# Optimization experiments

Measured on AMD Instinct MI355X. Metric: run time of the kernel, lower is better.

The kernel has to match this reference:

```python
import jax, jax.numpy as jnp
import numpy as np

N_NODES = 100000
N_EDGES = 1600000
NFEAT = 256
NHID = 128


def setup_inputs() -> dict:
    key = jax.random.key(0)
    ks = jax.random.split(key, 8)
    x = jax.random.normal(ks[0], (N_NODES, NFEAT), dtype=jnp.float32)
    edge_row = jax.random.randint(ks[1], (N_EDGES,), 0, N_NODES, dtype=jnp.int32)
    edge_col = jax.random.randint(ks[2], (N_EDGES,), 0, N_NODES, dtype=jnp.int32)
    edge_val = jax.random.uniform(ks[3], (N_EDGES,), dtype=jnp.float32)
    # Glorot-ish init for the two GraphConvolution weights
    W1 = jax.random.normal(ks[4], (NFEAT, NHID), dtype=jnp.float32) * (1.0 / np.sqrt(NFEAT))
    b1 = jnp.zeros((NHID,), dtype=jnp.float32)
    W2 = jax.random.normal(ks[5], (NHID, NHID), dtype=jnp.float32) * (1.0 / np.sqrt(NHID))
    b2 = jnp.zeros((NHID,), dtype=jnp.float32)
    return {"x": x, "edge_row": edge_row, "edge_col": edge_col,
            "edge_val": edge_val, "W1": W1, "b1": b1, "W2": W2, "b2": b2}


def _gcn_layer(h, W, b, edge_row, edge_col, edge_val, n_nodes):
    # support = h @ W  (dense transform), then spmm(adj, support) + b
    support = h @ W                              # [N, d_out]
    msgs = edge_val[:, None] * support[edge_col]  # [E, d_out] gather
    agg = jax.ops.segment_sum(msgs, edge_row, num_segments=n_nodes)  # scatter-add
    return agg + b


def reference(x, edge_row, edge_col, edge_val, W1, b1, W2, b2):
    n = x.shape[0]
    # eval mode: dropout is identity
    h = jax.nn.relu(_gcn_layer(x, W1, b1, edge_row, edge_col, edge_val, n))
    for _ in range(4):  # gc2 applied 4 times with shared weights
        h = jax.nn.relu(_gcn_layer(h, W2, b2, edge_row, edge_col, edge_val, n))
    return h
```

## Files before the change

kernel.cpp:

```cpp
#include <hip/hip_runtime.h>

constexpr int NFEAT = 256;
constexpr int NHID  = 128;
constexpr int SCAN_B = 4096;


__global__ void hist_kernel(const int* __restrict__ rows, int* __restrict__ cnt,
                            int* __restrict__ rank, int n) {
  int i = blockIdx.x * blockDim.x + threadIdx.x;
  if (i < n) rank[i] = atomicAdd(&cnt[rows[i]], 1);
}

__global__ void scan1_kernel(const int* __restrict__ cnt, int* __restrict__ part,
                             int* __restrict__ bsum, int n) {
  __shared__ int tmp[1024];
  int tid = threadIdx.x;
  int base = blockIdx.x * SCAN_B + tid * 4;
  int4 v = make_int4(0, 0, 0, 0);
  if (base + 4 <= n) {
    v = *(const int4*)&cnt[base];
  } else {
    if (base + 0 < n) v.x = cnt[base + 0];
    if (base + 1 < n) v.y = cnt[base + 1];
    if (base + 2 < n) v.z = cnt[base + 2];
    if (base + 3 < n) v.w = cnt[base + 3];
  }
  int s = v.x + v.y + v.z + v.w;
  tmp[tid] = s;
  __syncthreads();
  for (int off = 1; off < 1024; off <<= 1) {
    int t = (tid >= off) ? tmp[tid - off] : 0;
    __syncthreads();
    tmp[tid] += t;
    __syncthreads();
  }
  int excl = tmp[tid] - s;
  if (base + 0 < n) part[base + 0] = excl;
  if (base + 1 < n) part[base + 1] = excl + v.x;
  if (base + 2 < n) part[base + 2] = excl + v.x + v.y;
  if (base + 3 < n) part[base + 3] = excl + v.x + v.y + v.z;
  if (tid == 1023) bsum[blockIdx.x] = tmp[1023];
}

__global__ void scan2_kernel(int* __restrict__ bsum, int nb) {
  if (threadIdx.x == 0 && blockIdx.x == 0) {
    int run = 0;
    for (int i = 0; i < nb; ++i) { int t = bsum[i]; bsum[i] = run; run += t; }
    bsum[nb] = run;
  }
}

__global__ void scan3_kernel(int* __restrict__ row_ptr, const int* __restrict__ bsum,
                             int n, int nb) {
  int i = blockIdx.x * blockDim.x + threadIdx.x;
  if (i < n) row_ptr[i] += bsum[i / SCAN_B];
  if (i == 0) row_ptr[n] = bsum[nb];
}

__global__ void scatter_kernel(const int* __restrict__ rows, const int* __restrict__ cols,
                               const float* __restrict__ vals, const int* __restrict__ rank,
                               const int* __restrict__ row_ptr, int2* __restrict__ ev_s, int n) {
  int i = blockIdx.x * blockDim.x + threadIdx.x;
  if (i < n) {
    int p = row_ptr[rows[i]] + rank[i];
    ev_s[p] = make_int2(cols[i], __float_as_int(vals[i]));
  }
}


__device__ __forceinline__ void gload16(const float* src, float* dst_lds) {
  __builtin_amdgcn_global_load_lds(
      (const __attribute__((address_space(1))) void*)src,
      (__attribute__((address_space(3))) void*)dst_lds,
      16, 0, 0);
}

template<int K>
__global__ __launch_bounds__(256) void gemm_kernel(const float* __restrict__ A,
                                                   const float* __restrict__ W,
                                                   float* __restrict__ C, int M) {
  __shared__ __align__(16) float As[2][2048];
  __shared__ __align__(16) float Bs[2][2048];
  const int tid  = threadIdx.x;
  const int w    = tid >> 6;
  const int lane = tid & 63;
  const int r8   = tid >> 4;
  const int c8   = tid & 15;
  const int block_row = blockIdx.x * 128;

  float acc[2][2][4][4] = {};

  auto prefetch = [&](int t) {
    const int buf = t & 1;
    const int k0  = t * 16;
    #pragma unroll
    for (int j = 0; j < 2; ++j) {
      int s   = j * 256 + w * 64 + lane;
      int row = s >> 2;
      int q   = (s & 3) ^ ((row >> 2) & 3);
      int grow = block_row + row;
      if (grow >= M) grow = M - 1;
      gload16(A + (size_t)grow * K + k0 + q * 4,
              &As[buf][(j * 256 + w * 64) * 4]);
    }
    #pragma unroll
    for (int j = 0; j < 2; ++j) {
      int s = j * 256 + w * 64 + lane;
      int r = s >> 5, cq = s & 31;
      gload16(W + (size_t)(k0 + r) * 128 + cq * 4,
              &Bs[buf][(j * 256 + w * 64) * 4]);
    }
  };

  constexpr int NT = K / 16;
  prefetch(0);
  for (int t = 0; t < NT; ++t) {
    __syncthreads();
    if (t + 1 < NT) prefetch(t + 1);
    const float* as = As[t & 1];
    const float* bs = Bs[t & 1];
    #pragma unroll
    for (int q = 0; q < 4; ++q) {
      float av[2][4][4];
      #pragma unroll
      for (int rh = 0; rh < 2; ++rh)
        #pragma unroll
        for (int i = 0; i < 4; ++i) {
          int row = rh * 64 + r8 * 4 + i;
          float4 a = *(const float4*)&as[(row * 4 + (q ^ ((row >> 2) & 3))) * 4];
          av[rh][i][0] = a.x; av[rh][i][1] = a.y;
          av[rh][i][2] = a.z; av[rh][i][3] = a.w;
        }
      #pragma unroll
      for (int j = 0; j < 4; ++j) {
        int kk = q * 4 + j;
        float4 b0 = *(const float4*)&bs[(kk * 32 + c8) * 4];
        float4 b1 = *(const float4*)&bs[(kk * 32 + 16 + c8) * 4];
        #pragma unroll
        for (int rh = 0; rh < 2; ++rh)
          #pragma unroll
          for (int i = 0; i < 4; ++i) {
            float a = av[rh][i][j];
            acc[rh][0][i][0] += a * b0.x; acc[rh][0][i][1] += a * b0.y;
            acc[rh][0][i][2] += a * b0.z; acc[rh][0][i][3] += a * b0.w;
            acc[rh][1][i][0] += a * b1.x; acc[rh][1][i][1] += a * b1.y;
            acc[rh][1][i][2] += a * b1.z; acc[rh][1][i][3] += a * b1.w;
          }
      }
    }
  }

  #pragma unroll
  for (int rh = 0; rh < 2; ++rh)
    #pragma unroll
    for (int i = 0; i < 4; ++i) {
      int grow = block_row + rh * 64 + r8 * 4 + i;
      if (grow < M) {
        #pragma unroll
        for (int ch = 0; ch < 2; ++ch) {
          float4 v = make_float4(acc[rh][ch][i][0], acc[rh][ch][i][1],
                                 acc[rh][ch][i][2], acc[rh][ch][i][3]);
          *(float4*)&C[(size_t)grow * 128 + ch * 64 + c8 * 4] = v;
        }
      }
    }
}


__global__ void spmm_kernel(const float* __restrict__ support, const int* __restrict__ row_ptr,
                            const int2* __restrict__ ev, const float* __restrict__ bias,
                            float* __restrict__ out, int n_nodes) {
  int wid   = blockIdx.x * (blockDim.x >> 6) + (threadIdx.x >> 6);
  int lane  = threadIdx.x & 63;
  int half  = lane >> 5;
  int flane = lane & 31;
  int row   = wid * 2 + half;
  bool rv   = row < n_nodes;
  int beg = rv ? row_ptr[row]     : 0;
  int end = rv ? row_ptr[row + 1] : 0;
  int deg = end - beg;
  int mdeg = max(__shfl(deg, 0), __shfl(deg, 32));

  float4 acc = make_float4(0.f, 0.f, 0.f, 0.f);
  const int sb = half * 32;

  for (int chunk = 0; chunk < mdeg; chunk += 32) {
    int idx = beg + chunk + flane;
    int2 ee = (idx < end) ? ev[idx] : make_int2(0, 0);
    int   cl = ee.x;
    float vl = __int_as_float(ee.y);
    int m = min(32, mdeg - chunk);
    int e = 0;
    for (; e + 8 <= m; e += 8) {
      int   c0 = __shfl(cl, sb + e + 0), c1 = __shfl(cl, sb + e + 1);
      int   c2 = __shfl(cl, sb + e + 2), c3 = __shfl(cl, sb + e + 3);
      int   c4 = __shfl(cl, sb + e + 4), c5 = __shfl(cl, sb + e + 5);
      int   c6 = __shfl(cl, sb + e + 6), c7 = __shfl(cl, sb + e + 7);
      float v0 = __shfl(vl, sb + e + 0), v1 = __shfl(vl, sb + e + 1);
      float v2 = __shfl(vl, sb + e + 2), v3 = __shfl(vl, sb + e + 3);
      float v4 = __shfl(vl, sb + e + 4), v5 = __shfl(vl, sb + e + 5);
      float v6 = __shfl(vl, sb + e + 6), v7 = __shfl(vl, sb + e + 7);
      float4 s0 = *(const float4*)&support[(size_t)c0 * 128 + flane * 4];
      float4 s1 = *(const float4*)&support[(size_t)c1 * 128 + flane * 4];
      float4 s2 = *(const float4*)&support[(size_t)c2 * 128 + flane * 4];
      float4 s3 = *(const float4*)&support[(size_t)c3 * 128 + flane * 4];
      float4 s4 = *(const float4*)&support[(size_t)c4 * 128 + flane * 4];
      float4 s5 = *(const float4*)&support[(size_t)c5 * 128 + flane * 4];
      float4 s6 = *(const float4*)&support[(size_t)c6 * 128 + flane * 4];
      float4 s7 = *(const float4*)&support[(size_t)c7 * 128 + flane * 4];
      acc.x += v0 * s0.x; acc.y += v0 * s0.y; acc.z += v0 * s0.z; acc.w += v0 * s0.w;
      acc.x += v1 * s1.x; acc.y += v1 * s1.y; acc.z += v1 * s1.z; acc.w += v1 * s1.w;
      acc.x += v2 * s2.x; acc.y += v2 * s2.y; acc.z += v2 * s2.z; acc.w += v2 * s2.w;
      acc.x += v3 * s3.x; acc.y += v3 * s3.y; acc.z += v3 * s3.z; acc.w += v3 * s3.w;
      acc.x += v4 * s4.x; acc.y += v4 * s4.y; acc.z += v4 * s4.z; acc.w += v4 * s4.w;
      acc.x += v5 * s5.x; acc.y += v5 * s5.y; acc.z += v5 * s5.z; acc.w += v5 * s5.w;
      acc.x += v6 * s6.x; acc.y += v6 * s6.y; acc.z += v6 * s6.z; acc.w += v6 * s6.w;
      acc.x += v7 * s7.x; acc.y += v7 * s7.y; acc.z += v7 * s7.z; acc.w += v7 * s7.w;
    }
    for (; e < m; ++e) {
      int   ce = __shfl(cl, sb + e);
      float ve = __shfl(vl, sb + e);
      float4 s = *(const float4*)&support[(size_t)ce * 128 + flane * 4];
      acc.x += ve * s.x; acc.y += ve * s.y; acc.z += ve * s.z; acc.w += ve * s.w;
    }
  }
  if (rv) {
    float4 b = *(const float4*)&bias[flane * 4];
    float4 o = make_float4(fmaxf(acc.x + b.x, 0.f), fmaxf(acc.y + b.y, 0.f),
                           fmaxf(acc.z + b.z, 0.f), fmaxf(acc.w + b.w, 0.f));
    *(float4*)&out[(size_t)row * 128 + flane * 4] = o;
  }
}


extern "C" void kernel_launch(void* const* d_in, const int* in_sizes, int n_in,
                              void* d_out, int out_size, void* d_ws, size_t ws_size,
                              hipStream_t stream) {
  const float* x    = (const float*)d_in[0];
  const int*   erow = (const int*)d_in[1];
  const int*   ecol = (const int*)d_in[2];
  const float* evl  = (const float*)d_in[3];
  const float* W1   = (const float*)d_in[4];
  const float* b1   = (const float*)d_in[5];
  const float* W2   = (const float*)d_in[6];
  const float* b2   = (const float*)d_in[7];
  int n_nodes = in_sizes[0] / NFEAT;
  int n_edges = in_sizes[1];
  float* out = (float*)d_out;

  char* ws = (char*)d_ws;
  size_t off = 0;
  auto alloc = [&](size_t bytes) -> void* {
    void* p = ws + off;
    off += bytes;
    off = (off + 255) & ~(size_t)255;
    return p;
  };
  float* support = (float*)alloc((size_t)n_nodes * NHID * sizeof(float));
  int*   cnt     = (int*)alloc((size_t)n_nodes * sizeof(int));
  int*   row_ptr = (int*)alloc(((size_t)n_nodes + 1) * sizeof(int));
  int*   rank    = (int*)alloc((size_t)n_edges * sizeof(int));
  int2*  ev_s    = (int2*)alloc((size_t)n_edges * sizeof(int2));
  int nb = (n_nodes + SCAN_B - 1) / SCAN_B;
  int*   bsum    = (int*)alloc((size_t)(nb + 1) * sizeof(int));

  hipMemsetAsync(cnt, 0, (size_t)n_nodes * sizeof(int), stream);
  hist_kernel<<<(n_edges + 255) / 256, 256, 0, stream>>>(erow, cnt, rank, n_edges);
  scan1_kernel<<<nb, 1024, 0, stream>>>(cnt, row_ptr, bsum, n_nodes);
  scan2_kernel<<<1, 64, 0, stream>>>(bsum, nb);
  scan3_kernel<<<(n_nodes + 255) / 256, 256, 0, stream>>>(row_ptr, bsum, n_nodes, nb);
  scatter_kernel<<<(n_edges + 255) / 256, 256, 0, stream>>>(erow, ecol, evl, rank,
                                                            row_ptr, ev_s, n_edges);

  int gblocks = (n_nodes + 127) / 128;
  int sblocks = (n_nodes + 7) / 8;

  gemm_kernel<NFEAT><<<gblocks, 256, 0, stream>>>(x, W1, support, n_nodes);
  spmm_kernel<<<sblocks, 256, 0, stream>>>(support, row_ptr, ev_s, b1, out, n_nodes);

  for (int l = 0; l < 4; ++l) {
    gemm_kernel<NHID><<<gblocks, 256, 0, stream>>>(out, W2, support, n_nodes);
    spmm_kernel<<<sblocks, 256, 0, stream>>>(support, row_ptr, ev_s, b2, out, n_nodes);
  }
}
```

Baseline: 980.0 us.

## Sort rows by degree for balanced SpMM and unroll gather loop by 16

Adds a counting sort of rows by in-degree (histogram, reverse scan, scatter into a row permutation) so each wavefront's two half-wave rows have similar degree, which reduces divergence caused by padding to the larger degree. The SpMM kernel now reads its row through the permutation and gains a 16-wide unrolled gather loop to keep more loads in flight. The cost is three extra setup kernels, an extra indirection per row, and output writes and row_ptr reads that are no longer in row order. The wider unroll also raises register pressure.

```diff
diff --git a/kernel.cpp b/kernel.cpp
--- a/kernel.cpp
+++ b/kernel.cpp
@@ -3,6 +3,7 @@
 constexpr int NFEAT = 256;
 constexpr int NHID  = 128;
 constexpr int SCAN_B = 4096;
+constexpr int DBINS  = 256;
 
 
 __global__ void hist_kernel(const int* __restrict__ rows, int* __restrict__ cnt,
@@ -64,6 +65,43 @@
   if (i < n) {
     int p = row_ptr[rows[i]] + rank[i];
     ev_s[p] = make_int2(cols[i], __float_as_int(vals[i]));
+  }
+}
+
+
+__global__ void deg_hist_kernel(const int* __restrict__ deg, int* __restrict__ dbins, int n) {
+  __shared__ int h[DBINS];
+  int tid = threadIdx.x;
+  if (tid < DBINS) h[tid] = 0;
+  __syncthreads();
+  for (int i = blockIdx.x * blockDim.x + tid; i < n; i += gridDim.x * blockDim.x)
+    atomicAdd(&h[min(deg[i], DBINS - 1)], 1);
+  __syncthreads();
+  if (tid < DBINS) atomicAdd(&dbins[tid], h[tid]);
+}
+
+__global__ void deg_scan_kernel(const int* __restrict__ dbins, int* __restrict__ dcur) {
+  __shared__ int tmp[DBINS];
+  int tid = threadIdx.x;
+  int rb  = DBINS - 1 - tid;
+  int v = dbins[rb];
+  tmp[tid] = v;
+  __syncthreads();
+  for (int off = 1; off < DBINS; off <<= 1) {
+    int t = (tid >= off) ? tmp[tid - off] : 0;
+    __syncthreads();
+    tmp[tid] += t;
+    __syncthreads();
+  }
+  dcur[rb] = tmp[tid] - v;
+}
+
+__global__ void deg_scatter_kernel(const int* __restrict__ deg, int* __restrict__ dcur,
+                                   int* __restrict__ rowperm, int n) {
+  int i = blockIdx.x * blockDim.x + threadIdx.x;
+  if (i < n) {
+    int pos = atomicAdd(&dcur[min(deg[i], DBINS - 1)], 1);
+    rowperm[pos] = i;
   }
 }
 
@@ -168,17 +206,19 @@
 
 
 __global__ void spmm_kernel(const float* __restrict__ support, const int* __restrict__ row_ptr,
-                            const int2* __restrict__ ev, const float* __restrict__ bias,
-                            float* __restrict__ out, int n_nodes) {
+                            const int2* __restrict__ ev, const int* __restrict__ rowperm,
+                            const float* __restrict__ bias, float* __restrict__ out,
+                            int n_nodes) {
   int wid   = blockIdx.x * (blockDim.x >> 6) + (threadIdx.x >> 6);
   int lane  = threadIdx.x & 63;
   int half  = lane >> 5;
   int flane = lane & 31;
-  int row   = wid * 2 + half;
-  bool rv   = row < n_nodes;
+  int pidx  = wid * 2 + half;
+  bool rv   = pidx < n_nodes;
+  int row   = rv ? rowperm[pidx] : 0;
   int beg = rv ? row_ptr[row]     : 0;
   int end = rv ? row_ptr[row + 1] : 0;
-  int deg = end - beg;
+  int deg = rv ? (end - beg) : 0;
   int mdeg = max(__shfl(deg, 0), __shfl(deg, 32));
 
   float4 acc = make_float4(0.f, 0.f, 0.f, 0.f);
@@ -191,6 +231,56 @@
     float vl = __int_as_float(ee.y);
     int m = min(32, mdeg - chunk);
     int e = 0;
+    for (; e + 16 <= m; e += 16) {
+      int   c0 = __shfl(cl, sb + e + 0),  c1 = __shfl(cl, sb + e + 1);
+      int   c2 = __shfl(cl, sb + e + 2),  c3 = __shfl(cl, sb + e + 3);
+      int   c4 = __shfl(cl, sb + e + 4),  c5 = __shfl(cl, sb + e + 5);
+      int   c6 = __shfl(cl, sb + e + 6),  c7 = __shfl(cl, sb + e + 7);
+      int   c8 = __shfl(cl, sb + e + 8),  c9 = __shfl(cl, sb + e + 9);
+      int   cA = __shfl(cl, sb + e + 10), cB = __shfl(cl, sb + e + 11);
+      int   cC = __shfl(cl, sb + e + 12), cD = __shfl(cl, sb + e + 13);
+      int   cE = __shfl(cl, sb + e + 14), cF = __shfl(cl, sb + e + 15);
+      float v0 = __shfl(vl, sb + e + 0),  v1 = __shfl(vl, sb + e + 1);
+      float v2 = __shfl(vl, sb + e + 2),  v3 = __shfl(vl, sb + e + 3);
+      float v4 = __shfl(vl, sb + e + 4),  v5 = __shfl(vl, sb + e + 5);
+      float v6 = __shfl(vl, sb + e + 6),  v7 = __shfl(vl, sb + e + 7);
+      float v8 = __shfl(vl, sb + e + 8),  v9 = __shfl(vl, sb + e + 9);
+      float vA = __shfl(vl, sb + e + 10), vB = __shfl(vl, sb + e + 11);
+      float vC = __shfl(vl, sb + e + 12), vD = __shfl(vl, sb + e + 13);
+      float vE = __shfl(vl, sb + e + 14), vF = __shfl(vl, sb + e + 15);
+      float4 s0 = *(const float4*)&support[(size_t)c0 * 128 + flane * 4];
+      float4 s1 = *(const float4*)&support[(size_t)c1 * 128 + flane * 4];
+      float4 s2 = *(const float4*)&support[(size_t)c2 * 128 + flane * 4];
+      float4 s3 = *(const float4*)&support[(size_t)c3 * 128 + flane * 4];
+      float4 s4 = *(const float4*)&support[(size_t)c4 * 128 + flane * 4];
+      float4 s5 = *(const float4*)&support[(size_t)c5 * 128 + flane * 4];
+      float4 s6 = *(const float4*)&support[(size_t)c6 * 128 + flane * 4];
+      float4 s7 = *(const float4*)&support[(size_t)c7 * 128 + flane * 4];
+      float4 s8 = *(const float4*)&support[(size_t)c8 * 128 + flane * 4];
+      float4 s9 = *(const float4*)&support[(size_t)c9 * 128 + flane * 4];
+      float4 sA = *(const float4*)&support[(size_t)cA * 128 + flane * 4];
+      float4 sB = *(const float4*)&support[(size_t)cB * 128 + flane * 4];
+      float4 sC = *(const float4*)&support[(size_t)cC * 128 + flane * 4];
+      float4 sD = *(const float4*)&support[(size_t)cD * 128 + flane * 4];
+      float4 sE = *(const float4*)&support[(size_t)cE * 128 + flane * 4];
+      float4 sF = *(const float4*)&support[(size_t)cF * 128 + flane * 4];
+      acc.x += v0 * s0.x; acc.y += v0 * s0.y; acc.z += v0 * s0.z; acc.w += v0 * s0.w;
+      acc.x += v1 * s1.x; acc.y += v1 * s1.y; acc.z += v1 * s1.z; acc.w += v1 * s1.w;
+      acc.x += v2 * s2.x; acc.y += v2 * s2.y; acc.z += v2 * s2.z; acc.w += v2 * s2.w;
+      acc.x += v3 * s3.x; acc.y += v3 * s3.y; acc.z += v3 * s3.z; acc.w += v3 * s3.w;
+      acc.x += v4 * s4.x; acc.y += v4 * s4.y; acc.z += v4 * s4.z; acc.w += v4 * s4.w;
+      acc.x += v5 * s5.x; acc.y += v5 * s5.y; acc.z += v5 * s5.z; acc.w += v5 * s5.w;
+      acc.x += v6 * s6.x; acc.y += v6 * s6.y; acc.z += v6 * s6.z; acc.w += v6 * s6.w;
+      acc.x += v7 * s7.x; acc.y += v7 * s7.y; acc.z += v7 * s7.z; acc.w += v7 * s7.w;
+      acc.x += v8 * s8.x; acc.y += v8 * s8.y; acc.z += v8 * s8.z; acc.w += v8 * s8.w;
+      acc.x += v9 * s9.x; acc.y += v9 * s9.y; acc.z += v9 * s9.z; acc.w += v9 * s9.w;
+      acc.x += vA * sA.x; acc.y += vA * sA.y; acc.z += vA * sA.z; acc.w += vA * sA.w;
+      acc.x += vB * sB.x; acc.y += vB * sB.y; acc.z += vB * sB.z; acc.w += vB * sB.w;
+      acc.x += vC * sC.x; acc.y += vC * sC.y; acc.z += vC * sC.z; acc.w += vC * sC.w;
+      acc.x += vD * sD.x; acc.y += vD * sD.y; acc.z += vD * sD.z; acc.w += vD * sD.w;
+      acc.x += vE * sE.x; acc.y += vE * sE.y; acc.z += vE * sE.z; acc.w += vE * sE.w;
+      acc.x += vF * sF.x; acc.y += vF * sF.y; acc.z += vF * sF.z; acc.w += vF * sF.w;
+    }
     for (; e + 8 <= m; e += 8) {
       int   c0 = __shfl(cl, sb + e + 0), c1 = __shfl(cl, sb + e + 1);
       int   c2 = __shfl(cl, sb + e + 2), c3 = __shfl(cl, sb + e + 3);
@@ -261,25 +351,32 @@
   int*   row_ptr = (int*)alloc(((size_t)n_nodes + 1) * sizeof(int));
   int*   rank    = (int*)alloc((size_t)n_edges * sizeof(int));
   int2*  ev_s    = (int2*)alloc((size_t)n_edges * sizeof(int2));
+  int*   rowperm = (int*)alloc((size_t)n_nodes * sizeof(int));
+  int*   dbins   = (int*)alloc(DBINS * sizeof(int));
+  int*   dcur    = (int*)alloc(DBINS * sizeof(int));
   int nb = (n_nodes + SCAN_B - 1) / SCAN_B;
   int*   bsum    = (int*)alloc((size_t)(nb + 1) * sizeof(int));
 
   hipMemsetAsync(cnt, 0, (size_t)n_nodes * sizeof(int), stream);
+  hipMemsetAsync(dbins, 0, DBINS * sizeof(int), stream);
   hist_kernel<<<(n_edges + 255) / 256, 256, 0, stream>>>(erow, cnt, rank, n_edges);
   scan1_kernel<<<nb, 1024, 0, stream>>>(cnt, row_ptr, bsum, n_nodes);
   scan2_kernel<<<1, 64, 0, stream>>>(bsum, nb);
   scan3_kernel<<<(n_nodes + 255) / 256, 256, 0, stream>>>(row_ptr, bsum, n_nodes, nb);
   scatter_kernel<<<(n_edges + 255) / 256, 256, 0, stream>>>(erow, ecol, evl, rank,
                                                             row_ptr, ev_s, n_edges);
+  deg_hist_kernel<<<64, 256, 0, stream>>>(cnt, dbins, n_nodes);
+  deg_scan_kernel<<<1, DBINS, 0, stream>>>(dbins, dcur);
+  deg_scatter_kernel<<<(n_nodes + 255) / 256, 256, 0, stream>>>(cnt, dcur, rowperm, n_nodes);
 
   int gblocks = (n_nodes + 127) / 128;
   int sblocks = (n_nodes + 7) / 8;
 
   gemm_kernel<NFEAT><<<gblocks, 256, 0, stream>>>(x, W1, support, n_nodes);
-  spmm_kernel<<<sblocks, 256, 0, stream>>>(support, row_ptr, ev_s, b1, out, n_nodes);
+  spmm_kernel<<<sblocks, 256, 0, stream>>>(support, row_ptr, ev_s, rowperm, b1, out, n_nodes);
 
   for (int l = 0; l < 4; ++l) {
     gemm_kernel<NHID><<<gblocks, 256, 0, stream>>>(out, W2, support, n_nodes);
-    spmm_kernel<<<sblocks, 256, 0, stream>>>(support, row_ptr, ev_s, b2, out, n_nodes);
-  }
-}
+    spmm_kernel<<<sblocks, 256, 0, stream>>>(support, row_ptr, ev_s, rowperm, b2, out, n_nodes);
+  }
+}
```

Result: slower. 1.267 ms (+29.3%).
